# Kernel optimization log

Hardware: AMD Instinct MI355X
Metric: run time of the kernel (lower is better)

The kernel has to match this reference:

```python
import jax, jax.numpy as jnp
import numpy as np

K_NN = 2       # module's k (kNN count)
ALPHA = 1.1    # threshold = mean + alpha * std


def setup_inputs() -> dict:
    key = jax.random.key(0)
    x = jax.random.normal(key, (4, 8192, 3), dtype=jnp.float32)  # [B, K, 3]
    return {"x": x}


def reference(x):
    # Statistical outlier removal (SOR). Torch version runs the distance /
    # mask computation on a detached copy -> stop_gradient here.
    pc = jax.lax.stop_gradient(x)                      # [B, K, 3]
    xx = jnp.sum(pc * pc, axis=-1)                     # [B, K]
    # squared pairwise distances: ||a||^2 - 2 a.b + ||b||^2  -> [B, K, K]
    dist = xx[:, :, None] - 2.0 * jnp.einsum('bkd,bjd->bkj', pc, pc) + xx[:, None, :]
    # kNN distances: take k+1 smallest (incl. self at distance ~0), drop self
    neg_val, _ = jax.lax.top_k(-dist, K_NN + 1)        # [B, K, k+1]
    value = jnp.mean(-neg_val[..., 1:], axis=-1)       # [B, K] mean kNN dist
    mean = jnp.mean(value, axis=-1)                    # [B]
    std = jnp.std(value, axis=-1, ddof=1)              # [B] unbiased (torch.std)
    threshold = mean + ALPHA * std                     # [B]
    mask = value <= threshold[:, None]                 # [B, K] keep-mask
    # Torch returns a ragged list x[i][mask[i]]; for a jit-able fixed-shape
    # reference we return the masked (zero-padded) points plus the mask.
    masked_pc = x * mask[..., None].astype(x.dtype)    # [B, K, 3]
    return masked_pc, mask
```

## Files before the change

### kernel.cpp

```cpp
#include <hip/hip_runtime.h>
#include <math.h>


constexpr int B = 4;
constexpr int K = 8192;
constexpr int QPB = 256;
constexpr int QPT = 4;
constexpr int QBLK = QPB * QPT;

#define BIG 3.0e38f

using f32x16 = __attribute__((ext_vector_type(16))) float;

#define MINSERT(d, e0, e1, e2)                                  \
  do {                                                          \
    const float n0_ = fminf((e0), (d));                         \
    const float n1_ = __builtin_amdgcn_fmed3f((d), (e0), (e1)); \
    const float n2_ = __builtin_amdgcn_fmed3f((d), (e1), (e2)); \
    (e0) = n0_; (e1) = n1_; (e2) = n2_;                         \
  } while (0)

#define PQ1(PX, PY, PZ, PW, Q)                                        \
  do {                                                                \
    const float dot_ = (qx[Q] * (PX) + qy[Q] * (PY)) + qz[Q] * (PZ);  \
    const float d_ = (qn[Q] - 2.0f * dot_) + (PW);                    \
    MINSERT(d_, e0[Q], e1[Q], e2[Q]);                                 \
  } while (0)

__global__ __launch_bounds__(256) void pack_kernel(
    const float* __restrict__ x, float4* __restrict__ pack) {
  const int g = blockIdx.x * 256 + threadIdx.x;
  const float px = x[(size_t)g * 3 + 0];
  const float py = x[(size_t)g * 3 + 1];
  const float pz = x[(size_t)g * 3 + 2];
  pack[g] = make_float4(px, py, pz, (px * px + py * py) + pz * pz);
}

template <int CHUNK>
__global__ __launch_bounds__(QPB, 4) void knn_part_kernel(
    const float4* __restrict__ pack, float* __restrict__ part) {
  constexpr int NCH = K / CHUNK;
  const int bid   = blockIdx.x;
  const int chunk = bid % NCH;
  const int rest  = bid / NCH;
  const int kc    = rest % (K / QBLK);
  const int b     = rest / (K / QBLK);
  const int tid   = threadIdx.x;

  const float4* pb = pack + (size_t)b * K;

  float qx[QPT], qy[QPT], qz[QPT], qn[QPT];
#pragma unroll
  for (int q = 0; q < QPT; ++q) {
    const float4 f = pb[kc * QBLK + q * QPB + tid];
    qx[q] = f.x; qy[q] = f.y; qz[q] = f.z; qn[q] = f.w;
  }

  float e0[QPT], e1[QPT], e2[QPT];
#pragma unroll
  for (int q = 0; q < QPT; ++q) { e0[q] = BIG; e1[q] = BIG; e2[q] = BIG; }

  const float4* pp = pb + chunk * CHUNK;
  for (int j = 0; j < CHUNK; j += 8, pp += 8) {
    f32x16 c0, c1;
    asm volatile("s_load_dwordx16 %0, %1, 0x0" : "=s"(c0) : "s"(pp));
    asm volatile("s_load_dwordx16 %0, %1, 0x0" : "=s"(c1) : "s"(pp + 4));
    asm volatile("s_waitcnt lgkmcnt(0)" : "+s"(c0), "+s"(c1));
#pragma unroll
    for (int u = 0; u < 4; ++u) {
#pragma unroll
      for (int q = 0; q < QPT; ++q) {
        PQ1(c0[4 * u + 0], c0[4 * u + 1], c0[4 * u + 2], c0[4 * u + 3], q);
      }
    }
#pragma unroll
    for (int u = 0; u < 4; ++u) {
#pragma unroll
      for (int q = 0; q < QPT; ++q) {
        PQ1(c1[4 * u + 0], c1[4 * u + 1], c1[4 * u + 2], c1[4 * u + 3], q);
      }
    }
  }

#pragma unroll
  for (int q = 0; q < QPT; ++q) {
    const int k = kc * QBLK + q * QPB + tid;
    float* dst = part + ((size_t)chunk * (B * K) + (size_t)b * K + k) * 3;
    dst[0] = e0[q];
    dst[1] = e1[q];
    dst[2] = e2[q];
  }
}

template <int NCH>
__global__ __launch_bounds__(256) void sor_value_kernel(
    const float* __restrict__ part, float* __restrict__ value,
    double* __restrict__ bsum) {
  const int blk = blockIdx.x;
  const int b   = blk >> 5;
  const int tid = threadIdx.x;
  const int k   = (blk & 31) * 256 + tid;

  const float* pp = part + (size_t)(b * K + k) * 3;
  float d0 = BIG, d1 = BIG, d2 = BIG;
#pragma unroll 4
  for (int ch = 0; ch < NCH; ++ch) {
    const float a0 = pp[0];
    const float a1 = pp[1];
    const float a2 = pp[2];
    MINSERT(a0, d0, d1, d2);
    MINSERT(a1, d0, d1, d2);
    MINSERT(a2, d0, d1, d2);
    pp += (size_t)B * K * 3;
  }
  const float v = 0.5f * (d1 + d2);
  value[b * K + k] = v;

  double s = (double)v, s2 = (double)v * (double)v;
  for (int off = 32; off > 0; off >>= 1) {
    s  += __shfl_down(s, off, 64);
    s2 += __shfl_down(s2, off, 64);
  }
  __shared__ double rs[4], rs2[4];
  const int wave = tid >> 6;
  if ((tid & 63) == 0) { rs[wave] = s; rs2[wave] = s2; }
  __syncthreads();
  if (tid == 0) {
    double S = 0.0, S2 = 0.0;
    for (int w = 0; w < 4; ++w) { S += rs[w]; S2 += rs2[w]; }
    bsum[blk * 2 + 0] = S;
    bsum[blk * 2 + 1] = S2;
  }
}

__global__ __launch_bounds__(64) void sor_thresh_kernel(
    const double* __restrict__ bsum, float* __restrict__ thr) {
  const int b = threadIdx.x;
  if (b < B) {
    double S = 0.0, S2 = 0.0;
    for (int w = 0; w < 32; ++w) {
      S  += bsum[(b * 32 + w) * 2 + 0];
      S2 += bsum[(b * 32 + w) * 2 + 1];
    }
    const double mean = S / (double)K;
    const double var  = (S2 - S * S / (double)K) / (double)(K - 1);
    thr[b] = (float)(mean + 1.1 * sqrt(var));
  }
}

__global__ __launch_bounds__(256) void sor_mask_kernel(
    const float* __restrict__ x, const float* __restrict__ value,
    const float* __restrict__ thr, float* __restrict__ out) {
  const int g = blockIdx.x * 256 + threadIdx.x;
  const int b = g / K;
  const float m = (value[g] <= thr[b]) ? 1.0f : 0.0f;
  out[(size_t)B * K * 3 + g] = m;
  const size_t base = (size_t)g * 3;
  out[base + 0] = x[base + 0] * m;
  out[base + 1] = x[base + 1] * m;
  out[base + 2] = x[base + 2] * m;
}

template <int NCH>
static void run(const float* x, float* out, char* ws, hipStream_t stream) {
  float4* pack = (float4*)ws;
  size_t off = (size_t)B * K * sizeof(float4);
  float* part = (float*)(ws + off);
  off += (size_t)B * K * NCH * 3 * sizeof(float);
  float* value = (float*)(ws + off);
  off += (size_t)B * K * sizeof(float);
  off = (off + 7) & ~(size_t)7;
  double* bsum = (double*)(ws + off);
  off += (size_t)B * 32 * 2 * sizeof(double);
  float* thr = (float*)(ws + off);

  pack_kernel<<<B * K / 256, 256, 0, stream>>>(x, pack);
  knn_part_kernel<K / NCH><<<B * (K / QBLK) * NCH, QPB, 0, stream>>>(pack, part);
  sor_value_kernel<NCH><<<B * 32, 256, 0, stream>>>(part, value, bsum);
  sor_thresh_kernel<<<1, 64, 0, stream>>>(bsum, thr);
  sor_mask_kernel<<<B * K / 256, 256, 0, stream>>>(x, value, thr, out);
}

extern "C" void kernel_launch(void* const* d_in, const int* in_sizes, int n_in,
                              void* d_out, int out_size, void* d_ws, size_t ws_size,
                              hipStream_t stream) {
  const float* x = (const float*)d_in[0];
  float* out = (float*)d_out;
  char* ws = (char*)d_ws;

  const size_t fixed = (size_t)B * K * sizeof(float4) +
                       (size_t)B * K * sizeof(float) + 4096;
  if (ws_size >= (size_t)B * K * 32 * 3 * sizeof(float) + fixed) {
    run<32>(x, out, ws, stream);
  } else if (ws_size >= (size_t)B * K * 16 * 3 * sizeof(float) + fixed) {
    run<16>(x, out, ws, stream);
  } else if (ws_size >= (size_t)B * K * 8 * 3 * sizeof(float) + fixed) {
    run<8>(x, out, ws, stream);
  } else {
    run<2>(x, out, ws, stream);
  }
}
```

Before: 76.02 us.

## Use packed-FP32 distance math with SoA layout, double-buffered scalar loads, fused threshold

The pack buffer changes from AoS float4 to four SoA planes, so each iteration loads 8 candidates per coordinate with s_load_dwordx8. Distances are computed two candidates at a time with v_pk_mul/v_pk_fma/v_pk_add_f32 inline asm, keeping two top-3 lists per query that are merged at the end. Scalar loads are double-buffered so the next batch is fetched while the current one is computed. The threshold kernel is folded into the mask kernel, where each block recomputes the threshold into shared memory, which removes one launch. Costs include more VGPRs for the duplicated query pairs and the extra end-of-loop merge, and the NCH=16 workspace branch is dropped.

```diff
diff --git a/kernel.cpp b/kernel.cpp
--- a/kernel.cpp
+++ b/kernel.cpp
@@ -4,13 +4,14 @@
 
 constexpr int B = 4;
 constexpr int K = 8192;
+constexpr int BK = B * K;
 constexpr int QPB = 256;
 constexpr int QPT = 4;
 constexpr int QBLK = QPB * QPT;
 
 #define BIG 3.0e38f
 
-using f32x16 = __attribute__((ext_vector_type(16))) float;
+using f32x8 = __attribute__((ext_vector_type(8))) float;
 
 #define MINSERT(d, e0, e1, e2)                                  \
   do {                                                          \
@@ -20,26 +21,49 @@
     (e0) = n0_; (e1) = n1_; (e2) = n2_;                         \
   } while (0)
 
-#define PQ1(PX, PY, PZ, PW, Q)                                        \
-  do {                                                                \
-    const float dot_ = (qx[Q] * (PX) + qy[Q] * (PY)) + qz[Q] * (PZ);  \
-    const float d_ = (qn[Q] - 2.0f * dot_) + (PW);                    \
-    MINSERT(d_, e0[Q], e1[Q], e2[Q]);                                 \
+#define PK_DIST(DE, XP, YP, ZP, WP, Q)                                       \
+  float2 DE;                                                                 \
+  do {                                                                       \
+    float2 t0_, t1_, t2_, dd_;                                               \
+    asm("v_pk_mul_f32 %0, %1, %2" : "=v"(t0_) : "s"(XP), "v"(qx2[Q]));       \
+    asm("v_pk_fma_f32 %0, %1, %2, %3"                                        \
+        : "=v"(t1_) : "s"(YP), "v"(qy2[Q]), "v"(t0_));                       \
+    asm("v_pk_fma_f32 %0, %1, %2, %3"                                        \
+        : "=v"(t2_) : "s"(ZP), "v"(qz2[Q]), "v"(t1_));                       \
+    asm("v_pk_fma_f32 %0, %1, %2, %3"                                        \
+        : "=v"(dd_) : "v"(t2_), "v"(vm2), "v"(qn2[Q]));                      \
+    asm("v_pk_add_f32 %0, %1, %2" : "=v"(DE) : "s"(WP), "v"(dd_));           \
   } while (0)
 
 __global__ __launch_bounds__(256) void pack_kernel(
-    const float* __restrict__ x, float4* __restrict__ pack) {
+    const float* __restrict__ x, float* __restrict__ pack) {
   const int g = blockIdx.x * 256 + threadIdx.x;
   const float px = x[(size_t)g * 3 + 0];
   const float py = x[(size_t)g * 3 + 1];
   const float pz = x[(size_t)g * 3 + 2];
-  pack[g] = make_float4(px, py, pz, (px * px + py * py) + pz * pz);
-}
+  pack[0 * BK + g] = px;
+  pack[1 * BK + g] = py;
+  pack[2 * BK + g] = pz;
+  pack[3 * BK + g] = (px * px + py * py) + pz * pz;
+}
+
+#define ISSUE8(BX, BY, BZ, BW, PX, PY, PZ, PW)                         \
+  do {                                                                 \
+    asm volatile("s_load_dwordx8 %0, %1, 0x0" : "=s"(BX) : "s"(PX));   \
+    asm volatile("s_load_dwordx8 %0, %1, 0x0" : "=s"(BY) : "s"(PY));   \
+    asm volatile("s_load_dwordx8 %0, %1, 0x0" : "=s"(BZ) : "s"(PZ));   \
+    asm volatile("s_load_dwordx8 %0, %1, 0x0" : "=s"(BW) : "s"(PW));   \
+  } while (0)
+
+#define WAIT4(BX, BY, BZ, BW)                                          \
+  asm volatile("s_waitcnt lgkmcnt(0)"                                  \
+               : "+s"(BX), "+s"(BY), "+s"(BZ), "+s"(BW))
 
 template <int CHUNK>
 __global__ __launch_bounds__(QPB, 4) void knn_part_kernel(
-    const float4* __restrict__ pack, float* __restrict__ part) {
+    const float* __restrict__ pack, float* __restrict__ part) {
   constexpr int NCH = K / CHUNK;
+  constexpr int NIT = CHUNK / 8;
   const int bid   = blockIdx.x;
   const int chunk = bid % NCH;
   const int rest  = bid / NCH;
@@ -47,49 +71,82 @@
   const int b     = rest / (K / QBLK);
   const int tid   = threadIdx.x;
 
-  const float4* pb = pack + (size_t)b * K;
-
-  float qx[QPT], qy[QPT], qz[QPT], qn[QPT];
-#pragma unroll
-  for (int q = 0; q < QPT; ++q) {
-    const float4 f = pb[kc * QBLK + q * QPB + tid];
-    qx[q] = f.x; qy[q] = f.y; qz[q] = f.z; qn[q] = f.w;
-  }
-
-  float e0[QPT], e1[QPT], e2[QPT];
-#pragma unroll
-  for (int q = 0; q < QPT; ++q) { e0[q] = BIG; e1[q] = BIG; e2[q] = BIG; }
-
-  const float4* pp = pb + chunk * CHUNK;
-  for (int j = 0; j < CHUNK; j += 8, pp += 8) {
-    f32x16 c0, c1;
-    asm volatile("s_load_dwordx16 %0, %1, 0x0" : "=s"(c0) : "s"(pp));
-    asm volatile("s_load_dwordx16 %0, %1, 0x0" : "=s"(c1) : "s"(pp + 4));
-    asm volatile("s_waitcnt lgkmcnt(0)" : "+s"(c0), "+s"(c1));
-#pragma unroll
-    for (int u = 0; u < 4; ++u) {
-#pragma unroll
-      for (int q = 0; q < QPT; ++q) {
-        PQ1(c0[4 * u + 0], c0[4 * u + 1], c0[4 * u + 2], c0[4 * u + 3], q);
-      }
-    }
-#pragma unroll
-    for (int u = 0; u < 4; ++u) {
-#pragma unroll
-      for (int q = 0; q < QPT; ++q) {
-        PQ1(c1[4 * u + 0], c1[4 * u + 1], c1[4 * u + 2], c1[4 * u + 3], q);
-      }
-    }
-  }
-
+  const float* Xpl = pack + 0 * BK + b * K;
+  const float* Ypl = pack + 1 * BK + b * K;
+  const float* Zpl = pack + 2 * BK + b * K;
+  const float* Wpl = pack + 3 * BK + b * K;
+
+  float2 qx2[QPT], qy2[QPT], qz2[QPT], qn2[QPT];
 #pragma unroll
   for (int q = 0; q < QPT; ++q) {
     const int k = kc * QBLK + q * QPB + tid;
-    float* dst = part + ((size_t)chunk * (B * K) + (size_t)b * K + k) * 3;
-    dst[0] = e0[q];
-    dst[1] = e1[q];
-    dst[2] = e2[q];
-  }
+    const float qx = Xpl[k], qy = Ypl[k], qz = Zpl[k], qn = Wpl[k];
+    qx2[q] = make_float2(qx, qx);
+    qy2[q] = make_float2(qy, qy);
+    qz2[q] = make_float2(qz, qz);
+    qn2[q] = make_float2(qn, qn);
+  }
+  const float2 vm2 = make_float2(-2.0f, -2.0f);
+
+  float e0[QPT][2], e1[QPT][2], e2[QPT][2];
+#pragma unroll
+  for (int q = 0; q < QPT; ++q)
+#pragma unroll
+    for (int p = 0; p < 2; ++p) { e0[q][p] = BIG; e1[q][p] = BIG; e2[q][p] = BIG; }
+
+  const float* pX = Xpl + chunk * CHUNK;
+  const float* pY = Ypl + chunk * CHUNK;
+  const float* pZ = Zpl + chunk * CHUNK;
+  const float* pW = Wpl + chunk * CHUNK;
+
+  f32x8 ax, ay, az, aw, bx, by, bz, bw;
+
+#define COMPUTE8(BX, BY, BZ, BW)                                        \
+  do {                                                                  \
+    _Pragma("unroll")                                                   \
+    for (int p = 0; p < 4; ++p) {                                       \
+      const float2 Xp = make_float2((BX)[2 * p], (BX)[2 * p + 1]);      \
+      const float2 Yp = make_float2((BY)[2 * p], (BY)[2 * p + 1]);      \
+      const float2 Zp = make_float2((BZ)[2 * p], (BZ)[2 * p + 1]);      \
+      const float2 Wp = make_float2((BW)[2 * p], (BW)[2 * p + 1]);      \
+      _Pragma("unroll")                                                 \
+      for (int q = 0; q < QPT; ++q) {                                   \
+        PK_DIST(de, Xp, Yp, Zp, Wp, q);                                 \
+        MINSERT(de.x, e0[q][0], e1[q][0], e2[q][0]);                    \
+        MINSERT(de.y, e0[q][1], e1[q][1], e2[q][1]);                    \
+      }                                                                 \
+    }                                                                   \
+  } while (0)
+
+  ISSUE8(ax, ay, az, aw, pX, pY, pZ, pW);
+  for (int it = 0; it < NIT; it += 2) {
+    WAIT4(ax, ay, az, aw);
+    ISSUE8(bx, by, bz, bw, pX + 8, pY + 8, pZ + 8, pW + 8);
+    __builtin_amdgcn_sched_barrier(0);
+    COMPUTE8(ax, ay, az, aw);
+
+    WAIT4(bx, by, bz, bw);
+    if (it + 2 < NIT) {
+      ISSUE8(ax, ay, az, aw, pX + 16, pY + 16, pZ + 16, pW + 16);
+    }
+    __builtin_amdgcn_sched_barrier(0);
+    COMPUTE8(bx, by, bz, bw);
+
+    pX += 16; pY += 16; pZ += 16; pW += 16;
+  }
+
+#pragma unroll
+  for (int q = 0; q < QPT; ++q) {
+    MINSERT(e0[q][1], e0[q][0], e1[q][0], e2[q][0]);
+    MINSERT(e1[q][1], e0[q][0], e1[q][0], e2[q][0]);
+    MINSERT(e2[q][1], e0[q][0], e1[q][0], e2[q][0]);
+    const int k = kc * QBLK + q * QPB + tid;
+    float* dst = part + ((size_t)chunk * BK + (size_t)b * K + k) * 3;
+    dst[0] = e0[q][0];
+    dst[1] = e1[q][0];
+    dst[2] = e2[q][0];
+  }
+#undef COMPUTE8
 }
 
 template <int NCH>
@@ -111,7 +168,7 @@
     MINSERT(a0, d0, d1, d2);
     MINSERT(a1, d0, d1, d2);
     MINSERT(a2, d0, d1, d2);
-    pp += (size_t)B * K * 3;
+    pp += (size_t)BK * 3;
   }
   const float v = 0.5f * (d1 + d2);
   value[b * K + k] = v;
@@ -133,10 +190,14 @@
   }
 }
 
-__global__ __launch_bounds__(64) void sor_thresh_kernel(
-    const double* __restrict__ bsum, float* __restrict__ thr) {
-  const int b = threadIdx.x;
-  if (b < B) {
+__global__ __launch_bounds__(256) void sor_mask_kernel(
+    const float* __restrict__ x, const float* __restrict__ value,
+    const double* __restrict__ bsum, float* __restrict__ out) {
+  const int g = blockIdx.x * 256 + threadIdx.x;
+  const int b = g / K;
+
+  __shared__ float sthr;
+  if (threadIdx.x == 0) {
     double S = 0.0, S2 = 0.0;
     for (int w = 0; w < 32; ++w) {
       S  += bsum[(b * 32 + w) * 2 + 0];
@@ -144,17 +205,12 @@
     }
     const double mean = S / (double)K;
     const double var  = (S2 - S * S / (double)K) / (double)(K - 1);
-    thr[b] = (float)(mean + 1.1 * sqrt(var));
-  }
-}
-
-__global__ __launch_bounds__(256) void sor_mask_kernel(
-    const float* __restrict__ x, const float* __restrict__ value,
-    const float* __restrict__ thr, float* __restrict__ out) {
-  const int g = blockIdx.x * 256 + threadIdx.x;
-  const int b = g / K;
-  const float m = (value[g] <= thr[b]) ? 1.0f : 0.0f;
-  out[(size_t)B * K * 3 + g] = m;
+    sthr = (float)(mean + 1.1 * sqrt(var));
+  }
+  __syncthreads();
+
+  const float m = (value[g] <= sthr) ? 1.0f : 0.0f;
+  out[(size_t)BK * 3 + g] = m;
   const size_t base = (size_t)g * 3;
   out[base + 0] = x[base + 0] * m;
   out[base + 1] = x[base + 1] * m;
@@ -163,22 +219,19 @@
 
 template <int NCH>
 static void run(const float* x, float* out, char* ws, hipStream_t stream) {
-  float4* pack = (float4*)ws;
-  size_t off = (size_t)B * K * sizeof(float4);
+  float* pack = (float*)ws;
+  size_t off = (size_t)4 * BK * sizeof(float);
   float* part = (float*)(ws + off);
-  off += (size_t)B * K * NCH * 3 * sizeof(float);
+  off += (size_t)BK * NCH * 3 * sizeof(float);
   float* value = (float*)(ws + off);
-  off += (size_t)B * K * sizeof(float);
+  off += (size_t)BK * sizeof(float);
   off = (off + 7) & ~(size_t)7;
   double* bsum = (double*)(ws + off);
-  off += (size_t)B * 32 * 2 * sizeof(double);
-  float* thr = (float*)(ws + off);
-
-  pack_kernel<<<B * K / 256, 256, 0, stream>>>(x, pack);
+
+  pack_kernel<<<BK / 256, 256, 0, stream>>>(x, pack);
   knn_part_kernel<K / NCH><<<B * (K / QBLK) * NCH, QPB, 0, stream>>>(pack, part);
   sor_value_kernel<NCH><<<B * 32, 256, 0, stream>>>(part, value, bsum);
-  sor_thresh_kernel<<<1, 64, 0, stream>>>(bsum, thr);
-  sor_mask_kernel<<<B * K / 256, 256, 0, stream>>>(x, value, thr, out);
+  sor_mask_kernel<<<BK / 256, 256, 0, stream>>>(x, value, bsum, out);
 }
 
 extern "C" void kernel_launch(void* const* d_in, const int* in_sizes, int n_in,
@@ -188,13 +241,11 @@
   float* out = (float*)d_out;
   char* ws = (char*)d_ws;
 
-  const size_t fixed = (size_t)B * K * sizeof(float4) +
-                       (size_t)B * K * sizeof(float) + 4096;
-  if (ws_size >= (size_t)B * K * 32 * 3 * sizeof(float) + fixed) {
+  const size_t fixed = (size_t)4 * BK * sizeof(float) +
+                       (size_t)BK * sizeof(float) + 4096;
+  if (ws_size >= (size_t)BK * 32 * 3 * sizeof(float) + fixed) {
     run<32>(x, out, ws, stream);
-  } else if (ws_size >= (size_t)B * K * 16 * 3 * sizeof(float) + fixed) {
-    run<16>(x, out, ws, stream);
-  } else if (ws_size >= (size_t)B * K * 8 * 3 * sizeof(float) + fixed) {
+  } else if (ws_size >= (size_t)BK * 8 * 3 * sizeof(float) + fixed) {
     run<8>(x, out, ws, stream);
   } else {
     run<2>(x, out, ws, stream);
```

Result: faster. 73.90 us (-2.8%).
